# Optimization experiments

Measured on AMD Instinct MI355X. Metric: run time of the kernel, lower is better.

## Reference

```python
import jax, jax.numpy as jnp
import numpy as np

OUT_FEATURES = 8192
IN_FEATURES = 8192
BATCH = 512


def setup_inputs() -> dict:
    key = jax.random.key(0)
    k_x, k_w, k_s = jax.random.split(key, 3)
    x = jax.random.normal(k_x, (BATCH, IN_FEATURES), dtype=jnp.float32)
    # packed int4 weights: each int holds two nibbles (values 0..255)
    packed_weight = jax.random.randint(k_w, (OUT_FEATURES, IN_FEATURES // 2), 0, 256, dtype=jnp.int32)
    # per-output-row scale (positive, as produced by abs-max quantization)
    scale = jax.random.uniform(k_s, (OUT_FEATURES, 1), dtype=jnp.float32) * 0.02 + 1e-4
    return {"x": x, "packed_weight": packed_weight, "scale": scale}


def reference(x, packed_weight, scale):
    # Unpack two 4-bit values per byte: high nibble first (matches torch loop:
    # col i <- packed >> 4 & 15, col i+1 <- packed & 15), then subtract zero-point 8.
    hi = (packed_weight >> 4) & 15
    lo = packed_weight & 15
    q = jnp.stack([hi, lo], axis=-1).reshape(OUT_FEATURES, IN_FEATURES) - 8  # [out, in] int
    w = q.astype(scale.dtype) * scale  # dequantized weight [out, in]
    # linear: y = x @ W^T
    return jnp.einsum('bi,oi->bo', x, w)
```

## Files before the change

### kernel.cpp

```cpp
#include <hip/hip_runtime.h>
#include <cstdint>
#include <cstddef>

#define IN_F 8192
#define OUT_F 8192
#define BATCH 512
#define KSPLIT 4
#define KSLICE (IN_F / KSPLIT)
#define BK 32
#define NIT (KSLICE / BK)

typedef __bf16 bf16x8 __attribute__((ext_vector_type(8)));
typedef float floatx4 __attribute__((ext_vector_type(4)));

__device__ __forceinline__ ushort f2bf(float f) {
  uint32_t u = __float_as_uint(f);
  u += 0x7FFFu + ((u >> 16) & 1u);
  return (ushort)(u >> 16);
}

__device__ __forceinline__ uint32_t dq(int p) {
  uint32_t u = (uint32_t)p;
  return (((u >> 4) & 0xFu) | ((u & 0xFu) << 16)) | 0x43004300u;
}

__global__ __launch_bounds__(256) void cvt_rowsum(const float* __restrict__ x,
                                                  ushort* __restrict__ xb,
                                                  float* __restrict__ rowsum) {
  const int b = blockIdx.x;
  const int t = threadIdx.x;
  const float4* xr = (const float4*)(x + (size_t)b * IN_F);
  ushort4* xo = (ushort4*)(xb + (size_t)b * IN_F);
  float s[4] = {0.f, 0.f, 0.f, 0.f};
#pragma unroll
  for (int i = 0; i < 8; ++i) {
    float4 v = xr[i * 256 + t];
    ushort4 o;
    o.x = f2bf(v.x); o.y = f2bf(v.y); o.z = f2bf(v.z); o.w = f2bf(v.w);
    xo[i * 256 + t] = o;
    s[i >> 1] += __uint_as_float((uint32_t)o.x << 16) + __uint_as_float((uint32_t)o.y << 16)
               + __uint_as_float((uint32_t)o.z << 16) + __uint_as_float((uint32_t)o.w << 16);
  }
  __shared__ float red[4][4];
  const int lane = t & 63, wid = t >> 6;
#pragma unroll
  for (int j = 0; j < 4; ++j) {
    float v = s[j];
#pragma unroll
    for (int off = 32; off >= 1; off >>= 1) v += __shfl_down(v, off, 64);
    if (lane == 0) red[wid][j] = v;
  }
  __syncthreads();
  if (t < 4) rowsum[t * BATCH + b] = red[0][t] + red[1][t] + red[2][t] + red[3][t];
}

__global__ __launch_bounds__(256, 2) void qgemm(const ushort* __restrict__ xb,
                                                const int* __restrict__ pw,
                                                const float* __restrict__ scale,
                                                const float* __restrict__ rowsum,
                                                float* __restrict__ out) {
  __shared__ uint32_t As[2 * 128 * 16];
  __shared__ uint32_t Bs[2 * 128 * 16];

  const int tid = threadIdx.x;
  const int lane = tid & 63;
  const int w = tid >> 6;
  const int wm = w & 1, wn = w >> 1;
  const int lr = lane & 15, lq = lane >> 4;

  const int n0 = blockIdx.x * 128;
  const int m0 = blockIdx.y * 128;
  const int ks = blockIdx.z;

  const int r = tid >> 1, h = tid & 1;
  const char* aG = (const char*)xb + (size_t)(m0 + r) * (IN_F * 2) + ks * (KSLICE * 2) + h * 32;
  const char* bG = (const char*)pw + (size_t)(n0 + r) * (IN_F * 2) + ks * (KSLICE * 2) + h * 32;

  uint32_t* aW = As + r * 16 + h * 8;
  uint32_t* bW = Bs + r * 16 + h * 8;
  const uint32_t* aR = As + (wm * 64 + lr) * 16 + lq * 4;
  const uint32_t* bR = Bs + (wn * 64 + lr) * 16 + lq * 4;

  floatx4 acc[4][4] = {};

  int4 pa0 = *(const int4*)(aG);
  int4 pa1 = *(const int4*)(aG + 16);
  int4 pb0 = *(const int4*)(bG);
  int4 pb1 = *(const int4*)(bG + 16);
  aG += 64; bG += 64;

  for (int it = 0; it < NIT; ++it) {
    const int off = (it & 1) * (128 * 16);
    *(int4*)(aW + off) = pa0;
    *(int4*)(aW + off + 4) = pa1;
    int4 u0, u1;
    u0.x = dq(pb0.x); u0.y = dq(pb0.y); u0.z = dq(pb0.z); u0.w = dq(pb0.w);
    u1.x = dq(pb1.x); u1.y = dq(pb1.y); u1.z = dq(pb1.z); u1.w = dq(pb1.w);
    *(int4*)(bW + off) = u0;
    *(int4*)(bW + off + 4) = u1;
    __syncthreads();
    if (it + 1 < NIT) {
      pa0 = *(const int4*)(aG);
      pa1 = *(const int4*)(aG + 16);
      pb0 = *(const int4*)(bG);
      pb1 = *(const int4*)(bG + 16);
      aG += 64; bG += 64;
    }
    bf16x8 av[4], bv[4];
#pragma unroll
    for (int i = 0; i < 4; ++i) av[i] = *(const bf16x8*)(aR + off + i * 256);
#pragma unroll
    for (int i = 0; i < 4; ++i) bv[i] = *(const bf16x8*)(bR + off + i * 256);
#pragma unroll
    for (int mi = 0; mi < 4; ++mi)
#pragma unroll
      for (int ni = 0; ni < 4; ++ni)
        acc[mi][ni] = __builtin_amdgcn_mfma_f32_16x16x32_bf16(av[mi], bv[ni],
                                                              acc[mi][ni], 0, 0, 0);
  }

  const int om = m0 + wm * 64 + lq * 4;
  const int on = n0 + wn * 64 + lr;
  float scv[4];
#pragma unroll
  for (int ni = 0; ni < 4; ++ni) scv[ni] = scale[on + ni * 16];
  float rsv[4][4];
#pragma unroll
  for (int mi = 0; mi < 4; ++mi)
#pragma unroll
    for (int rr = 0; rr < 4; ++rr)
      rsv[mi][rr] = rowsum[ks * BATCH + om + mi * 16 + rr];

#pragma unroll
  for (int mi = 0; mi < 4; ++mi)
#pragma unroll
    for (int ni = 0; ni < 4; ++ni) {
      const float s = scv[ni];
      float* op = out + (size_t)(om + mi * 16) * OUT_F + (on + ni * 16);
#pragma unroll
      for (int rr = 0; rr < 4; ++rr)
        atomicAdd(op + (size_t)rr * OUT_F, s * (acc[mi][ni][rr] - 136.f * rsv[mi][rr]));
    }
}

extern "C" void kernel_launch(void* const* d_in, const int* in_sizes, int n_in,
                              void* d_out, int out_size, void* d_ws, size_t ws_size,
                              hipStream_t stream) {
  const float* x = (const float*)d_in[0];
  const int* pw = (const int*)d_in[1];
  const float* scale = (const float*)d_in[2];
  float* out = (float*)d_out;

  ushort* xb = (ushort*)d_ws;
  float* rowsum = (float*)((char*)d_ws + (size_t)BATCH * IN_F * sizeof(ushort));

  cvt_rowsum<<<BATCH, 256, 0, stream>>>(x, xb, rowsum);
  hipMemsetAsync(out, 0, (size_t)out_size * sizeof(float), stream);
  dim3 grid(OUT_F / 128, BATCH / 128, KSPLIT);
  qgemm<<<grid, 256, 0, stream>>>(xb, pw, scale, rowsum, out);
}
```

Baseline: 309.5 us.

## Load activations directly to registers and store packed int4 weights in LDS

Activation fragments now go straight from global memory into registers, double-buffered, so the A tile no longer passes through LDS. Weights are repacked into one byte per pair of nibbles in LDS and unpacked to bf16 with byte-permute instructions after the LDS read. This makes the LDS footprint much smaller, and the occupancy hint is raised from 2 to 3 blocks. The cost is uncoalesced, redundant global reads of A across the two N-warps, extra ALU work for the perm unpack in the inner loop, and higher register pressure.

Measured after the change: 366.7 us. +18.5%, slower.

```diff
diff --git a/kernel.cpp b/kernel.cpp
--- a/kernel.cpp
+++ b/kernel.cpp
@@ -19,9 +19,24 @@
   return (ushort)(u >> 16);
 }
 
-__device__ __forceinline__ uint32_t dq(int p) {
-  uint32_t u = (uint32_t)p;
-  return (((u >> 4) & 0xFu) | ((u & 0xFu) << 16)) | 0x43004300u;
+__device__ __forceinline__ uint32_t perm(uint32_t a, uint32_t b, uint32_t s) {
+  return __builtin_amdgcn_perm(a, b, s);
+}
+
+__device__ __forceinline__ bf16x8 unpack8(uint32_t u) {
+  uint32_t hi = (u >> 4) & 0x0F0F0F0Fu;
+  uint32_t lo = u & 0x0F0F0F0Fu;
+  uint32_t hl0 = perm(hi, lo, 0x01050004u);
+  uint32_t hl1 = perm(hi, lo, 0x03070206u);
+  const uint32_t c43 = 0x43434343u;
+  uint4 d;
+  d.x = perm(hl0, c43, 0x00050004u);
+  d.y = perm(hl0, c43, 0x00070006u);
+  d.z = perm(hl1, c43, 0x00050004u);
+  d.w = perm(hl1, c43, 0x00070006u);
+  union { uint4 u4; bf16x8 v; } cv;
+  cv.u4 = d;
+  return cv.v;
 }
 
 __global__ __launch_bounds__(256) void cvt_rowsum(const float* __restrict__ x,
@@ -54,13 +69,12 @@
   if (t < 4) rowsum[t * BATCH + b] = red[0][t] + red[1][t] + red[2][t] + red[3][t];
 }
 
-__global__ __launch_bounds__(256, 2) void qgemm(const ushort* __restrict__ xb,
+__global__ __launch_bounds__(256, 3) void qgemm(const ushort* __restrict__ xb,
                                                 const int* __restrict__ pw,
                                                 const float* __restrict__ scale,
                                                 const float* __restrict__ rowsum,
                                                 float* __restrict__ out) {
-  __shared__ uint32_t As[2 * 128 * 16];
-  __shared__ uint32_t Bs[2 * 128 * 16];
+  __shared__ uint32_t Bs[2 * 128 * 4];
 
   const int tid = threadIdx.x;
   const int lane = tid & 63;
@@ -72,50 +86,60 @@
   const int m0 = blockIdx.y * 128;
   const int ks = blockIdx.z;
 
+  const char* xbb = (const char*)xb;
+  uint32_t aoff[4];
+#pragma unroll
+  for (int mi = 0; mi < 4; ++mi)
+    aoff[mi] = (uint32_t)((m0 + wm * 64 + mi * 16 + lr) * (IN_F * 2) + ks * (KSLICE * 2) + lq * 16);
+
   const int r = tid >> 1, h = tid & 1;
-  const char* aG = (const char*)xb + (size_t)(m0 + r) * (IN_F * 2) + ks * (KSLICE * 2) + h * 32;
-  const char* bG = (const char*)pw + (size_t)(n0 + r) * (IN_F * 2) + ks * (KSLICE * 2) + h * 32;
-
-  uint32_t* aW = As + r * 16 + h * 8;
-  uint32_t* bW = Bs + r * 16 + h * 8;
-  const uint32_t* aR = As + (wm * 64 + lr) * 16 + lq * 4;
-  const uint32_t* bR = Bs + (wn * 64 + lr) * 16 + lq * 4;
+  const char* bgp = (const char*)pw + (size_t)(n0 + r) * (IN_F * 2) + ks * (KSLICE * 2) + h * 32;
+  uint32_t* bw = Bs + r * 4 + h * 2;
+  const uint32_t* brd = Bs + (wn * 64 + lr) * 4 + lq;
 
   floatx4 acc[4][4] = {};
 
-  int4 pa0 = *(const int4*)(aG);
-  int4 pa1 = *(const int4*)(aG + 16);
-  int4 pb0 = *(const int4*)(bG);
-  int4 pb1 = *(const int4*)(bG + 16);
-  aG += 64; bG += 64;
+  int4 p0 = *(const int4*)(bgp);
+  int4 p1 = *(const int4*)(bgp + 16);
+  bgp += 64;
+  bf16x8 av[2][4];
+#pragma unroll
+  for (int mi = 0; mi < 4; ++mi) {
+    av[0][mi] = *(const bf16x8*)(xbb + aoff[mi]);
+    aoff[mi] += 64;
+  }
 
+#pragma unroll 2
   for (int it = 0; it < NIT; ++it) {
-    const int off = (it & 1) * (128 * 16);
-    *(int4*)(aW + off) = pa0;
-    *(int4*)(aW + off + 4) = pa1;
-    int4 u0, u1;
-    u0.x = dq(pb0.x); u0.y = dq(pb0.y); u0.z = dq(pb0.z); u0.w = dq(pb0.w);
-    u1.x = dq(pb1.x); u1.y = dq(pb1.y); u1.z = dq(pb1.z); u1.w = dq(pb1.w);
-    *(int4*)(bW + off) = u0;
-    *(int4*)(bW + off + 4) = u1;
+    const int cur = it & 1;
+    uint32_t q0 = perm((uint32_t)p0.y, (uint32_t)p0.x, 0x00000400u);
+    uint32_t q1 = perm((uint32_t)p0.w, (uint32_t)p0.z, 0x00000400u);
+    uint32_t q2 = perm((uint32_t)p1.y, (uint32_t)p1.x, 0x00000400u);
+    uint32_t q3 = perm((uint32_t)p1.w, (uint32_t)p1.z, 0x00000400u);
+    uint2 dd;
+    dd.x = perm(q1, q0, 0x05040100u);
+    dd.y = perm(q3, q2, 0x05040100u);
+    *(uint2*)(bw + cur * 512) = dd;
     __syncthreads();
     if (it + 1 < NIT) {
-      pa0 = *(const int4*)(aG);
-      pa1 = *(const int4*)(aG + 16);
-      pb0 = *(const int4*)(bG);
-      pb1 = *(const int4*)(bG + 16);
-      aG += 64; bG += 64;
+      p0 = *(const int4*)(bgp);
+      p1 = *(const int4*)(bgp + 16);
+      bgp += 64;
+#pragma unroll
+      for (int mi = 0; mi < 4; ++mi) {
+        av[cur ^ 1][mi] = *(const bf16x8*)(xbb + aoff[mi]);
+        aoff[mi] += 64;
+      }
     }
-    bf16x8 av[4], bv[4];
+    const uint32_t* brc = brd + cur * 512;
+    bf16x8 bv[4];
 #pragma unroll
-    for (int i = 0; i < 4; ++i) av[i] = *(const bf16x8*)(aR + off + i * 256);
-#pragma unroll
-    for (int i = 0; i < 4; ++i) bv[i] = *(const bf16x8*)(bR + off + i * 256);
+    for (int ni = 0; ni < 4; ++ni) bv[ni] = unpack8(brc[ni * 64]);
 #pragma unroll
     for (int mi = 0; mi < 4; ++mi)
 #pragma unroll
       for (int ni = 0; ni < 4; ++ni)
-        acc[mi][ni] = __builtin_amdgcn_mfma_f32_16x16x32_bf16(av[mi], bv[ni],
+        acc[mi][ni] = __builtin_amdgcn_mfma_f32_16x16x32_bf16(av[cur][mi], bv[ni],
                                                               acc[mi][ni], 0, 0, 0);
   }
 
```
